# Optimization experiments

Measured on AMD Instinct MI355X. Metric: run time of the kernel, lower is better.

Reference implementation:

```python
import jax, jax.numpy as jnp
import numpy as np

# Model config (matches init_kwargs)
DIM = 2048
INTER = 1408          # moe_inter_dim
E = 16                # n_routed_experts
TOPK = 4              # n_activated_experts
G = 4                 # n_expert_groups
TOPK_G = 2            # n_limited_groups
N_SHARED = 2
SHARED_INTER = N_SHARED * INTER  # 2816
ROUTE_SCALE = 1.0


def setup_inputs() -> dict:
    key = jax.random.key(0)
    ks = jax.random.split(key, 8)
    s = 0.02
    x = jax.random.normal(ks[0], (1, 2048, DIM), dtype=jnp.float32)
    Wg = jax.random.normal(ks[1], (E, DIM), dtype=jnp.float32) * s      # gate weight
    W1 = jax.random.normal(ks[2], (E, INTER, DIM), dtype=jnp.float32) * s  # expert gate proj
    W3 = jax.random.normal(ks[3], (E, INTER, DIM), dtype=jnp.float32) * s  # expert up proj
    W2 = jax.random.normal(ks[4], (E, DIM, INTER), dtype=jnp.float32) * s  # expert down proj
    Ws1 = jax.random.normal(ks[5], (SHARED_INTER, DIM), dtype=jnp.float32) * s
    Ws3 = jax.random.normal(ks[6], (SHARED_INTER, DIM), dtype=jnp.float32) * s
    Ws2 = jax.random.normal(ks[7], (DIM, SHARED_INTER), dtype=jnp.float32) * s
    return {"x": x, "Wg": Wg, "W1": W1, "W3": W3, "W2": W2,
            "Ws1": Ws1, "Ws3": Ws3, "Ws2": Ws2}


def _moe_forward(x, Wg, W1, W3, W2, Ws1, Ws3, Ws2):
    B, S, D = x.shape
    xt = x.reshape(-1, D)              # [T, D]
    T = xt.shape[0]

    # ---- Gate: group-limited top-k routing (bias is None since dim != 7168) ----
    scores = jax.nn.softmax(xt @ Wg.T, axis=-1)          # [T, E]
    sg = scores.reshape(T, G, E // G)                    # [T, G, E/G]
    group_scores = sg.max(axis=-1)                       # amax per group
    gidx = jax.lax.top_k(group_scores, TOPK_G)[1]        # [T, TOPK_G]
    gmask = jax.nn.one_hot(gidx, G, dtype=jnp.float32).sum(axis=1) > 0  # [T, G] kept groups
    masked = jnp.where(gmask[:, :, None], sg, -jnp.inf).reshape(T, E)
    topi = jax.lax.top_k(masked, TOPK)[1]                # [T, TOPK] expert indices
    weights = jnp.take_along_axis(scores, topi, axis=1) * ROUTE_SCALE  # original_scores gather

    # ---- Routed experts: dense per-expert SwiGLU FFN, zero-weight combine ----
    # combine[t, e] = sum over k of weights[t, k] * (topi[t, k] == e)
    combine = jnp.zeros((T, E), xt.dtype).at[jnp.arange(T)[:, None], topi].add(weights)
    h = jax.nn.silu(jnp.einsum('td,eid->eti', xt, W1)) * jnp.einsum('td,eid->eti', xt, W3)
    expert_out = jnp.einsum('eti,edi->etd', h, W2)       # [E, T, D]
    y = jnp.einsum('etd,te->td', expert_out, combine)    # [T, D]

    # ---- Shared expert (applied to all tokens) ----
    z = (jax.nn.silu(xt @ Ws1.T) * (xt @ Ws3.T)) @ Ws2.T

    return (y + z).reshape(B, S, D)


def reference(x, Wg, W1, W3, W2, Ws1, Ws3, Ws2):
    return _moe_forward(x, Wg, W1, W3, W2, Ws1, Ws3, Ws2)
```

## Files before the change

kernel.cpp:

```cpp
#include <hip/hip_runtime.h>
#include <stdint.h>

#define D_MODEL  2048
#define N_INTER  1408
#define SH_INTER 2816
#define T_TOK    2048
#define NSLOT    (T_TOK * 4)
#define MIB(x)   ((size_t)(x) << 20)

typedef __attribute__((ext_vector_type(8))) short bf16x8;
typedef __attribute__((ext_vector_type(4))) float f32x4;

__device__ __forceinline__ unsigned short f2bf(float f){
  unsigned int b = __builtin_bit_cast(unsigned int, f);
  b = (b + 0x7FFFu + ((b >> 16) & 1u)) >> 16;
  return (unsigned short)b;
}
__device__ __forceinline__ float bf2f(unsigned short h){
  unsigned int b = ((unsigned int)h) << 16;
  return __builtin_bit_cast(float, b);
}

#define GLOAD16(gp, lp) __builtin_amdgcn_global_load_lds( \
    (const __attribute__((address_space(1))) unsigned int*)(gp), \
    (__attribute__((address_space(3))) unsigned int*)(lp), 16, 0, 0)

__global__ void cvt_bf16_kernel(const float* __restrict__ x,
                                unsigned short* __restrict__ o, int n4){
  const int stride = gridDim.x * blockDim.x;
  for (int i = blockIdx.x * blockDim.x + threadIdx.x; i < n4; i += stride){
    const float4 v = ((const float4*)x)[i];
    ushort4 u; u.x = f2bf(v.x); u.y = f2bf(v.y); u.z = f2bf(v.z); u.w = f2bf(v.w);
    ((ushort4*)o)[i] = u;
  }
}

__global__ void gate_kernel(const float* __restrict__ x, const float* __restrict__ Wg,
                            int* __restrict__ cnt, int* __restrict__ list,
                            float* __restrict__ wslot){
  const int t = blockIdx.x;
  const int l = threadIdx.x;
  const int e = l & 15, q = l >> 4;
  const float* xr = x + (size_t)t * D_MODEL + q * 512;
  const float* wr = Wg + (size_t)e * D_MODEL + q * 512;
  float p = 0.f;
  #pragma unroll 4
  for (int i = 0; i < 512; i += 4){
    float4 xv = *(const float4*)(xr + i);
    float4 wv = *(const float4*)(wr + i);
    p += xv.x*wv.x + xv.y*wv.y + xv.z*wv.z + xv.w*wv.w;
  }
  p += __shfl_xor(p, 16);
  p += __shfl_xor(p, 32);
  float mx = p;
  for (int d = 1; d < 16; d <<= 1) mx = fmaxf(mx, __shfl_xor(mx, d));
  float ex = __expf(p - mx);
  float sum = ex;
  for (int d = 1; d < 16; d <<= 1) sum += __shfl_xor(sum, d);
  const float sc = ex / sum;
  float gm = fmaxf(sc, __shfl_xor(sc, 1));
  gm = fmaxf(gm, __shfl_xor(gm, 2));
  const float g0 = __shfl(gm, 0), g1 = __shfl(gm, 4),
              g2 = __shfl(gm, 8), g3 = __shfl(gm, 12);
  const int grp = e >> 2;
  const float gs[4] = {g0, g1, g2, g3};
  int grank = 0;
  #pragma unroll
  for (int j = 0; j < 4; ++j)
    if (gs[j] > gm || (gs[j] == gm && j < grp)) grank++;
  const float msc = (grank < 2) ? sc : -INFINITY;
  int erank = 0;
  #pragma unroll
  for (int j = 0; j < 16; ++j){
    const float oj = __shfl(msc, j);
    if (oj > msc || (oj == msc && j < e)) erank++;
  }
  if (q == 0 && erank < 4 && msc > -INFINITY){
    const int pos = atomicAdd(&cnt[e], 1);
    const int slot = (t << 2) | erank;
    list[e * T_TOK + pos] = slot;
    wslot[slot] = sc;
  }
}

template<int MODE>
__global__ __launch_bounds__(256, 3)
void gemm6_kernel(const unsigned short* __restrict__ A,
                  const unsigned short* __restrict__ B,
                  void* __restrict__ OutP,
                  const int* __restrict__ list,
                  const int* __restrict__ cnt,
                  int N, int K, int Astride, int MT, int NT)
{
  constexpr bool GATHER = (MODE >= 2);
  __shared__ unsigned short As[3 * 128 * 32];
  __shared__ unsigned short Bs[3 * 128 * 32];

  const int per = gridDim.x >> 3;
  const int gsw = (blockIdx.x & 7) * per + (blockIdx.x >> 3);
  const int mt   = gsw % MT;
  const int rest = gsw / MT;
  const int nt = GATHER ? (rest % NT) : rest;
  const int e  = GATHER ? (rest / NT) : 0;

  const int cntE = GATHER ? cnt[e] : (MT * 128);
  if (mt * 128 >= cntE) return;

  const int tid = threadIdx.x, wid = tid >> 6, lane = tid & 63;

  const int rt0 = 32 * wid + (lane >> 2), rt1 = rt0 + 16;
  const int sxA = ((lane & 3) ^ ((lane >> 3) & 3)) << 3;

  int ar0, ar1;
  if constexpr (GATHER){
    const int lim = cntE - 1;
    int p0 = mt * 128 + rt0; p0 = p0 < lim ? p0 : lim;
    int p1 = mt * 128 + rt1; p1 = p1 < lim ? p1 : lim;
    const int e0 = list[e * T_TOK + p0], e1 = list[e * T_TOK + p1];
    ar0 = (MODE == 2) ? (e0 >> 2) : e0;
    ar1 = (MODE == 2) ? (e1 >> 2) : e1;
  } else { ar0 = mt * 128 + rt0; ar1 = mt * 128 + rt1; }

  const unsigned short* pa0 = A + (size_t)ar0 * Astride + sxA;
  const unsigned short* pa1 = A + (size_t)ar1 * Astride + sxA;
  const unsigned short* pb0 = B + (GATHER ? (size_t)e * N * K : 0)
                            + (size_t)(nt * 128 + rt0) * K + sxA;
  const unsigned short* pb1 = pb0 + (size_t)16 * K;

  const int aW0 = (32 * wid) * 32, aW1 = aW0 + 16 * 32;
  const int bufStride = 128 * 32;

  const int wr = wid >> 1, wc = wid & 1, lr = lane & 15, lq = lane >> 4;
  const int fx = ((lq ^ ((lr >> 1) & 3)) << 3);
  int aoff[4], boff[4];
  #pragma unroll
  for (int m = 0; m < 4; ++m) aoff[m] = (wr * 64 + m * 16 + lr) * 32 + fx;
  #pragma unroll
  for (int n = 0; n < 4; ++n) boff[n] = (wc * 64 + n * 16 + lr) * 32 + fx;

  f32x4 acc[4][4];
  const f32x4 zero = {0.f, 0.f, 0.f, 0.f};
  #pragma unroll
  for (int m = 0; m < 4; ++m)
    #pragma unroll
    for (int n = 0; n < 4; ++n) acc[m][n] = zero;

  const int KT = K >> 5;
  #pragma unroll
  for (int t = 0; t < 3; ++t){
    GLOAD16(pa0, As + t * bufStride + aW0);
    GLOAD16(pa1, As + t * bufStride + aW1);
    GLOAD16(pb0, Bs + t * bufStride + aW0);
    GLOAD16(pb1, Bs + t * bufStride + aW1);
    pa0 += 32; pa1 += 32; pb0 += 32; pb1 += 32;
  }
  int c = 0;

  for (int kt = 0; kt < KT; ++kt){
    if (kt < KT - 2)       asm volatile("s_waitcnt vmcnt(8)" ::: "memory");
    else if (kt == KT - 2) asm volatile("s_waitcnt vmcnt(4)" ::: "memory");
    else                   asm volatile("s_waitcnt vmcnt(0)" ::: "memory");
    __builtin_amdgcn_s_barrier();

    const unsigned short* aC = As + c * bufStride;
    const unsigned short* bC = Bs + c * bufStride;
    bf16x8 af[4], bf[4];
    #pragma unroll
    for (int m = 0; m < 4; ++m) af[m] = *(const bf16x8*)(aC + aoff[m]);
    #pragma unroll
    for (int n = 0; n < 4; ++n) bf[n] = *(const bf16x8*)(bC + boff[n]);

    asm volatile("s_waitcnt lgkmcnt(0)" ::: "memory");
    __builtin_amdgcn_sched_barrier(0);
    __builtin_amdgcn_s_barrier();

    if (kt + 3 < KT){
      GLOAD16(pa0, As + c * bufStride + aW0);
      GLOAD16(pa1, As + c * bufStride + aW1);
      GLOAD16(pb0, Bs + c * bufStride + aW0);
      GLOAD16(pb1, Bs + c * bufStride + aW1);
      pa0 += 32; pa1 += 32; pb0 += 32; pb1 += 32;
    }

    #pragma unroll
    for (int n = 0; n < 4; ++n)
      #pragma unroll
      for (int m = 0; m < 4; ++m)
        acc[m][n] = __builtin_amdgcn_mfma_f32_16x16x32_bf16(af[m], bf[n], acc[m][n], 0, 0, 0);

    c = (c == 2) ? 0 : c + 1;
  }

  const int colBase = nt * 128 + wc * 64;
  #pragma unroll
  for (int m = 0; m < 4; ++m){
    #pragma unroll
    for (int r = 0; r < 4; ++r){
      const int grow = mt * 128 + wr * 64 + m * 16 + lq * 4 + r;
      if constexpr (MODE == 1){
        float* op = (float*)OutP + (size_t)grow * N + colBase;
        #pragma unroll
        for (int n = 0; n < 4; ++n) op[n * 16 + lr] = acc[m][n][r];
      } else if constexpr (MODE == 0){
        unsigned short* op = (unsigned short*)OutP + (size_t)grow * N + colBase;
        #pragma unroll
        for (int n = 0; n < 4; ++n) op[n * 16 + lr] = f2bf(acc[m][n][r]);
      } else {
        if (grow >= cntE) continue;
        const int orow = list[e * T_TOK + grow];
        unsigned short* op = (unsigned short*)OutP + (size_t)orow * N + colBase;
        #pragma unroll
        for (int n = 0; n < 4; ++n) op[n * 16 + lr] = f2bf(acc[m][n][r]);
      }
    }
  }
}

__global__ void swiglu_ip_kernel(unsigned short* __restrict__ GU, int n8, int NI8){
  const int stride = gridDim.x * blockDim.x;
  bf16x8* p = (bf16x8*)GU;
  for (int i = blockIdx.x * blockDim.x + threadIdx.x; i < n8; i += stride){
    const int r = i / NI8, ccol = i - r * NI8;
    const size_t gi = (size_t)r * 2 * NI8 + ccol;
    const bf16x8 g = p[gi];
    const bf16x8 u = p[gi + NI8];
    bf16x8 h;
    #pragma unroll
    for (int j = 0; j < 8; ++j){
      const float gv = bf2f((unsigned short)g[j]);
      const float uv = bf2f((unsigned short)u[j]);
      h[j] = (short)f2bf(gv / (1.f + __expf(-gv)) * uv);
    }
    p[gi] = h;
  }
}

__global__ void swiglu2_kernel(unsigned short* __restrict__ G,
                               const unsigned short* __restrict__ U, int n8){
  const int stride = gridDim.x * blockDim.x;
  for (int i = blockIdx.x * blockDim.x + threadIdx.x; i < n8; i += stride){
    const bf16x8 g = ((const bf16x8*)G)[i];
    const bf16x8 u = ((const bf16x8*)U)[i];
    bf16x8 h;
    #pragma unroll
    for (int j = 0; j < 8; ++j){
      const float gv = bf2f((unsigned short)g[j]);
      const float uv = bf2f((unsigned short)u[j]);
      h[j] = (short)f2bf(gv / (1.f + __expf(-gv)) * uv);
    }
    ((bf16x8*)G)[i] = h;
  }
}

__global__ void combine_kernel(const unsigned short* __restrict__ H2,
                               const float* __restrict__ wslot,
                               float* __restrict__ out){
  const int t = blockIdx.x;
  const int ccol = threadIdx.x * 8;
  float w[4];
  #pragma unroll
  for (int k = 0; k < 4; ++k) w[k] = wslot[t * 4 + k];
  float* o = out + (size_t)t * D_MODEL + ccol;
  float a[8];
  #pragma unroll
  for (int j = 0; j < 8; ++j) a[j] = o[j];
  #pragma unroll
  for (int k = 0; k < 4; ++k){
    const bf16x8 hv = *(const bf16x8*)(H2 + (size_t)(t * 4 + k) * D_MODEL + ccol);
    #pragma unroll
    for (int j = 0; j < 8; ++j) a[j] += w[k] * bf2f((unsigned short)hv[j]);
  }
  #pragma unroll
  for (int j = 0; j < 8; ++j) o[j] = a[j];
}

extern "C" void kernel_launch(void* const* d_in, const int* in_sizes, int n_in,
                              void* d_out, int out_size, void* d_ws, size_t ws_size,
                              hipStream_t stream)
{
  const float* x   = (const float*)d_in[0];
  const float* Wg  = (const float*)d_in[1];
  const float* W1  = (const float*)d_in[2];
  const float* W3  = (const float*)d_in[3];
  const float* W2  = (const float*)d_in[4];
  const float* Ws1 = (const float*)d_in[5];
  const float* Ws3 = (const float*)d_in[6];
  const float* Ws2 = (const float*)d_in[7];
  float* out = (float*)d_out;

  char* ws = (char*)d_ws;
  int*   cnt   = (int*)(ws);
  int*   list  = (int*)(ws + 4096);
  float* wslot = (float*)(ws + 4096 + 131072);
  unsigned short* xbf  = (unsigned short*)(ws + MIB(1));
  unsigned short* H2   = (unsigned short*)(ws + MIB(1));
  unsigned short* GU_s = (unsigned short*)(ws + MIB(9));
  unsigned short* Ubuf = (unsigned short*)(ws + MIB(9));
  unsigned short* Wb   = (unsigned short*)(ws + MIB(33));
  unsigned short* Gbuf = (unsigned short*)(ws + MIB(121));
  unsigned short* Wb2  = Wb + (size_t)SH_INTER * D_MODEL;

  hipMemsetAsync(cnt, 0, 4096, stream);
  cvt_bf16_kernel<<<2048, 256, 0, stream>>>(x, xbf, T_TOK * D_MODEL / 4);
  gate_kernel<<<T_TOK, 64, 0, stream>>>(x, Wg, cnt, list, wslot);

  cvt_bf16_kernel<<<4096, 256, 0, stream>>>(Ws1, Wb,  SH_INTER * D_MODEL / 4);
  cvt_bf16_kernel<<<4096, 256, 0, stream>>>(Ws3, Wb2, SH_INTER * D_MODEL / 4);
  gemm6_kernel<0><<<16 * 44, 256, 0, stream>>>(xbf, Wb, GU_s, nullptr, nullptr,
                                               2 * SH_INTER, D_MODEL, D_MODEL, 16, 44);
  swiglu_ip_kernel<<<2048, 256, 0, stream>>>(GU_s, T_TOK * SH_INTER / 8, SH_INTER / 8);
  cvt_bf16_kernel<<<4096, 256, 0, stream>>>(Ws2, Wb, D_MODEL * SH_INTER / 4);
  gemm6_kernel<1><<<16 * 16, 256, 0, stream>>>(GU_s, Wb, out, nullptr, nullptr,
                                               D_MODEL, SH_INTER, 2 * SH_INTER, 16, 16);

  cvt_bf16_kernel<<<8192, 256, 0, stream>>>(W1, Wb, 16 * N_INTER * D_MODEL / 4);
  gemm6_kernel<2><<<16 * 11 * 16, 256, 0, stream>>>(xbf, Wb, Gbuf, list, cnt,
                                                    N_INTER, D_MODEL, D_MODEL, 16, 11);
  cvt_bf16_kernel<<<8192, 256, 0, stream>>>(W3, Wb, 16 * N_INTER * D_MODEL / 4);
  gemm6_kernel<2><<<16 * 11 * 16, 256, 0, stream>>>(xbf, Wb, Ubuf, list, cnt,
                                                    N_INTER, D_MODEL, D_MODEL, 16, 11);
  swiglu2_kernel<<<2048, 256, 0, stream>>>(Gbuf, Ubuf, NSLOT * N_INTER / 8);
  cvt_bf16_kernel<<<8192, 256, 0, stream>>>(W2, Wb, 16 * D_MODEL * N_INTER / 4);
  gemm6_kernel<3><<<16 * 16 * 16, 256, 0, stream>>>(Gbuf, Wb, H2, list, cnt,
                                                    D_MODEL, N_INTER, N_INTER, 16, 16);
  combine_kernel<<<T_TOK, 256, 0, stream>>>(H2, wslot, out);
}
```

Measured before the change: 604.5 us.

## Fuse gate/up GEMMs with SwiGLU epilogue and widen GEMM N-tiles to 256

Adds a gate/up GEMM kernel in which each block computes matching 128-column tiles of both the gate and up projections. The up tile is exchanged through shared memory and SiLU(g)*u is applied in the epilogue, so the separate SwiGLU kernels and the intermediate G/U buffer round trips go away. The down-projection GEMM now uses 128x256 tiles with 8 MFMA columns per wave. Routed expert weights are converted in two halves of 8 experts so W1 and W3 can sit in the workspace together. This raises register and LDS use per block (launch bounds drop to 2 blocks per CU) and halves the grid sizes, which may hurt occupancy and tail balance.

```diff
diff --git a/kernel.cpp b/kernel.cpp
--- a/kernel.cpp
+++ b/kernel.cpp
@@ -83,18 +83,169 @@
   }
 }
 
-template<int MODE>
-__global__ __launch_bounds__(256, 3)
-void gemm6_kernel(const unsigned short* __restrict__ A,
-                  const unsigned short* __restrict__ B,
-                  void* __restrict__ OutP,
-                  const int* __restrict__ list,
-                  const int* __restrict__ cnt,
-                  int N, int K, int Astride, int MT, int NT)
+template<int GATHER>
+__global__ __launch_bounds__(256, 2)
+void gemm_gu_kernel(const unsigned short* __restrict__ A,
+                    const unsigned short* __restrict__ BG,
+                    const unsigned short* __restrict__ BU,
+                    unsigned short* __restrict__ H,
+                    const int* __restrict__ list,
+                    const int* __restrict__ cnt,
+                    int ebase, int K, int NI, int MT, int NT)
 {
-  constexpr bool GATHER = (MODE >= 2);
-  __shared__ unsigned short As[3 * 128 * 32];
-  __shared__ unsigned short Bs[3 * 128 * 32];
+  __shared__ __align__(128) char smem[24576 + 49152];
+  unsigned short* As = (unsigned short*)smem;
+  unsigned short* Bs = (unsigned short*)(smem + 24576);
+  float* scr = (float*)smem;
+
+  const int per = gridDim.x >> 3;
+  const int gsw = (blockIdx.x & 7) * per + (blockIdx.x >> 3);
+  const int mt   = gsw % MT;
+  const int rest = gsw / MT;
+  const int nt = GATHER ? (rest % NT) : rest;
+  const int e  = GATHER ? (ebase + rest / NT) : 0;
+  const int cntE = GATHER ? cnt[e] : (MT * 128);
+  if (mt * 128 >= cntE) return;
+
+  const int tid = threadIdx.x, wid = tid >> 6, lane = tid & 63;
+  const int sx = ((lane & 3) ^ ((lane >> 3) & 3)) << 3;
+
+  const int rt0 = 32 * wid + (lane >> 2), rt1 = rt0 + 16;
+  int ar0, ar1;
+  if (GATHER){
+    const int lim = cntE - 1;
+    int p0 = mt * 128 + rt0; p0 = p0 < lim ? p0 : lim;
+    int p1 = mt * 128 + rt1; p1 = p1 < lim ? p1 : lim;
+    ar0 = list[e * T_TOK + p0] >> 2;
+    ar1 = list[e * T_TOK + p1] >> 2;
+  } else { ar0 = mt * 128 + rt0; ar1 = mt * 128 + rt1; }
+  const unsigned short* pa0 = A + (size_t)ar0 * K + sx;
+  const unsigned short* pa1 = A + (size_t)ar1 * K + sx;
+
+  const unsigned short* wsrc = (wid < 2) ? BG : BU;
+  if (GATHER) wsrc += (size_t)(e - ebase) * NI * K;
+  const int rb = (64 * wid + (lane >> 2)) & 127;
+  const unsigned short* pb0 = wsrc + (size_t)(nt * 128 + rb     ) * K + sx;
+  const unsigned short* pb1 = wsrc + (size_t)(nt * 128 + rb + 16) * K + sx;
+  const unsigned short* pb2 = wsrc + (size_t)(nt * 128 + rb + 32) * K + sx;
+  const unsigned short* pb3 = wsrc + (size_t)(nt * 128 + rb + 48) * K + sx;
+
+  const int aW0 = (32 * wid) * 32, aW1 = aW0 + 512;
+  const int bW  = (64 * wid) * 32;
+  const int aStr = 128 * 32, bStr = 256 * 32;
+
+  const int wr = wid >> 1, wc = wid & 1, lr = lane & 15, lq = lane >> 4;
+  const int fx = ((lq ^ ((lr >> 1) & 3)) << 3);
+  int aoff[4], boff[8];
+  #pragma unroll
+  for (int m = 0; m < 4; ++m) aoff[m] = (wr * 64 + m * 16 + lr) * 32 + fx;
+  #pragma unroll
+  for (int n = 0; n < 8; ++n) boff[n] = (wc * 128 + n * 16 + lr) * 32 + fx;
+
+  f32x4 acc[4][8];
+  const f32x4 zero = {0.f, 0.f, 0.f, 0.f};
+  #pragma unroll
+  for (int m = 0; m < 4; ++m)
+    #pragma unroll
+    for (int n = 0; n < 8; ++n) acc[m][n] = zero;
+
+  const int KT = K >> 5;
+  #pragma unroll
+  for (int t = 0; t < 3; ++t){
+    GLOAD16(pa0, As + t * aStr + aW0);
+    GLOAD16(pa1, As + t * aStr + aW1);
+    GLOAD16(pb0, Bs + t * bStr + bW);
+    GLOAD16(pb1, Bs + t * bStr + bW + 512);
+    GLOAD16(pb2, Bs + t * bStr + bW + 1024);
+    GLOAD16(pb3, Bs + t * bStr + bW + 1536);
+    pa0 += 32; pa1 += 32; pb0 += 32; pb1 += 32; pb2 += 32; pb3 += 32;
+  }
+  int c = 0;
+
+  for (int kt = 0; kt < KT; ++kt){
+    if (kt < KT - 2)       asm volatile("s_waitcnt vmcnt(12)" ::: "memory");
+    else if (kt == KT - 2) asm volatile("s_waitcnt vmcnt(6)"  ::: "memory");
+    else                   asm volatile("s_waitcnt vmcnt(0)"  ::: "memory");
+    __builtin_amdgcn_s_barrier();
+
+    const unsigned short* aC = As + c * aStr;
+    const unsigned short* bC = Bs + c * bStr;
+    bf16x8 af[4], bf[8];
+    #pragma unroll
+    for (int m = 0; m < 4; ++m) af[m] = *(const bf16x8*)(aC + aoff[m]);
+    #pragma unroll
+    for (int n = 0; n < 8; ++n) bf[n] = *(const bf16x8*)(bC + boff[n]);
+
+    asm volatile("s_waitcnt lgkmcnt(0)" ::: "memory");
+    __builtin_amdgcn_sched_barrier(0);
+    __builtin_amdgcn_s_barrier();
+
+    if (kt + 3 < KT){
+      GLOAD16(pa0, As + c * aStr + aW0);
+      GLOAD16(pa1, As + c * aStr + aW1);
+      GLOAD16(pb0, Bs + c * bStr + bW);
+      GLOAD16(pb1, Bs + c * bStr + bW + 512);
+      GLOAD16(pb2, Bs + c * bStr + bW + 1024);
+      GLOAD16(pb3, Bs + c * bStr + bW + 1536);
+      pa0 += 32; pa1 += 32; pb0 += 32; pb1 += 32; pb2 += 32; pb3 += 32;
+    }
+
+    #pragma unroll
+    for (int n = 0; n < 8; ++n)
+      #pragma unroll
+      for (int m = 0; m < 4; ++m)
+        acc[m][n] = __builtin_amdgcn_mfma_f32_16x16x32_bf16(af[m], bf[n], acc[m][n], 0, 0, 0);
+
+    c = (c == 2) ? 0 : c + 1;
+  }
+
+  if (wc == 1){
+    #pragma unroll
+    for (int m = 0; m < 4; ++m)
+      #pragma unroll
+      for (int r = 0; r < 4; ++r){
+        const int row = m * 16 + lq * 4 + r;
+        #pragma unroll
+        for (int n = 0; n < 8; ++n){
+          const int ucol = (n * 16 + lr) ^ ((lq & 1) << 4);
+          scr[wr * 8192 + row * 128 + ucol] = acc[m][n][r];
+        }
+      }
+  }
+  __syncthreads();
+  if (wc == 0){
+    #pragma unroll
+    for (int m = 0; m < 4; ++m)
+      #pragma unroll
+      for (int r = 0; r < 4; ++r){
+        const int row = m * 16 + lq * 4 + r;
+        const int grow = mt * 128 + wr * 64 + row;
+        if (GATHER && grow >= cntE) continue;
+        const int orow = GATHER ? list[e * T_TOK + grow] : grow;
+        unsigned short* op = H + (size_t)orow * NI + nt * 128;
+        #pragma unroll
+        for (int n = 0; n < 8; ++n){
+          const float g = acc[m][n][r];
+          const int ucol = (n * 16 + lr) ^ ((lq & 1) << 4);
+          const float u = scr[wr * 8192 + row * 128 + ucol];
+          op[n * 16 + lr] = f2bf(g / (1.f + __expf(-g)) * u);
+        }
+      }
+  }
+}
+
+template<int GATHER>
+__global__ __launch_bounds__(256, 2)
+void gemm_down_kernel(const unsigned short* __restrict__ A,
+                      const unsigned short* __restrict__ B,
+                      void* __restrict__ OutP,
+                      const int* __restrict__ list,
+                      const int* __restrict__ cnt,
+                      int K, int N, int MT, int NT)
+{
+  __shared__ __align__(128) char smem[24576 + 49152];
+  unsigned short* As = (unsigned short*)smem;
+  unsigned short* Bs = (unsigned short*)(smem + 24576);
 
   const int per = gridDim.x >> 3;
   const int gsw = (blockIdx.x & 7) * per + (blockIdx.x >> 3);
@@ -102,88 +253,93 @@
   const int rest = gsw / MT;
   const int nt = GATHER ? (rest % NT) : rest;
   const int e  = GATHER ? (rest / NT) : 0;
-
   const int cntE = GATHER ? cnt[e] : (MT * 128);
   if (mt * 128 >= cntE) return;
 
   const int tid = threadIdx.x, wid = tid >> 6, lane = tid & 63;
+  const int sx = ((lane & 3) ^ ((lane >> 3) & 3)) << 3;
 
   const int rt0 = 32 * wid + (lane >> 2), rt1 = rt0 + 16;
-  const int sxA = ((lane & 3) ^ ((lane >> 3) & 3)) << 3;
-
   int ar0, ar1;
-  if constexpr (GATHER){
+  if (GATHER){
     const int lim = cntE - 1;
     int p0 = mt * 128 + rt0; p0 = p0 < lim ? p0 : lim;
     int p1 = mt * 128 + rt1; p1 = p1 < lim ? p1 : lim;
-    const int e0 = list[e * T_TOK + p0], e1 = list[e * T_TOK + p1];
-    ar0 = (MODE == 2) ? (e0 >> 2) : e0;
-    ar1 = (MODE == 2) ? (e1 >> 2) : e1;
+    ar0 = list[e * T_TOK + p0];
+    ar1 = list[e * T_TOK + p1];
   } else { ar0 = mt * 128 + rt0; ar1 = mt * 128 + rt1; }
-
-  const unsigned short* pa0 = A + (size_t)ar0 * Astride + sxA;
-  const unsigned short* pa1 = A + (size_t)ar1 * Astride + sxA;
-  const unsigned short* pb0 = B + (GATHER ? (size_t)e * N * K : 0)
-                            + (size_t)(nt * 128 + rt0) * K + sxA;
-  const unsigned short* pb1 = pb0 + (size_t)16 * K;
-
-  const int aW0 = (32 * wid) * 32, aW1 = aW0 + 16 * 32;
-  const int bufStride = 128 * 32;
+  const unsigned short* pa0 = A + (size_t)ar0 * K + sx;
+  const unsigned short* pa1 = A + (size_t)ar1 * K + sx;
+
+  const unsigned short* wsrc = B + (GATHER ? (size_t)e * N * K : 0);
+  const int rb = 64 * wid + (lane >> 2);
+  const unsigned short* pb0 = wsrc + (size_t)(nt * 256 + rb     ) * K + sx;
+  const unsigned short* pb1 = wsrc + (size_t)(nt * 256 + rb + 16) * K + sx;
+  const unsigned short* pb2 = wsrc + (size_t)(nt * 256 + rb + 32) * K + sx;
+  const unsigned short* pb3 = wsrc + (size_t)(nt * 256 + rb + 48) * K + sx;
+
+  const int aW0 = (32 * wid) * 32, aW1 = aW0 + 512;
+  const int bW  = (64 * wid) * 32;
+  const int aStr = 128 * 32, bStr = 256 * 32;
 
   const int wr = wid >> 1, wc = wid & 1, lr = lane & 15, lq = lane >> 4;
   const int fx = ((lq ^ ((lr >> 1) & 3)) << 3);
-  int aoff[4], boff[4];
+  int aoff[4], boff[8];
   #pragma unroll
   for (int m = 0; m < 4; ++m) aoff[m] = (wr * 64 + m * 16 + lr) * 32 + fx;
   #pragma unroll
-  for (int n = 0; n < 4; ++n) boff[n] = (wc * 64 + n * 16 + lr) * 32 + fx;
-
-  f32x4 acc[4][4];
+  for (int n = 0; n < 8; ++n) boff[n] = (wc * 128 + n * 16 + lr) * 32 + fx;
+
+  f32x4 acc[4][8];
   const f32x4 zero = {0.f, 0.f, 0.f, 0.f};
   #pragma unroll
   for (int m = 0; m < 4; ++m)
     #pragma unroll
-    for (int n = 0; n < 4; ++n) acc[m][n] = zero;
+    for (int n = 0; n < 8; ++n) acc[m][n] = zero;
 
   const int KT = K >> 5;
   #pragma unroll
   for (int t = 0; t < 3; ++t){
-    GLOAD16(pa0, As + t * bufStride + aW0);
-    GLOAD16(pa1, As + t * bufStride + aW1);
-    GLOAD16(pb0, Bs + t * bufStride + aW0);
-    GLOAD16(pb1, Bs + t * bufStride + aW1);
-    pa0 += 32; pa1 += 32; pb0 += 32; pb1 += 32;
+    GLOAD16(pa0, As + t * aStr + aW0);
+    GLOAD16(pa1, As + t * aStr + aW1);
+    GLOAD16(pb0, Bs + t * bStr + bW);
+    GLOAD16(pb1, Bs + t * bStr + bW + 512);
+    GLOAD16(pb2, Bs + t * bStr + bW + 1024);
+    GLOAD16(pb3, Bs + t * bStr + bW + 1536);
+    pa0 += 32; pa1 += 32; pb0 += 32; pb1 += 32; pb2 += 32; pb3 += 32;
   }
   int c = 0;
 
   for (int kt = 0; kt < KT; ++kt){
-    if (kt < KT - 2)       asm volatile("s_waitcnt vmcnt(8)" ::: "memory");
-    else if (kt == KT - 2) asm volatile("s_waitcnt vmcnt(4)" ::: "memory");
-    else                   asm volatile("s_waitcnt vmcnt(0)" ::: "memory");
+    if (kt < KT - 2)       asm volatile("s_waitcnt vmcnt(12)" ::: "memory");
+    else if (kt == KT - 2) asm volatile("s_waitcnt vmcnt(6)"  ::: "memory");
+    else                   asm volatile("s_waitcnt vmcnt(0)"  ::: "memory");
     __builtin_amdgcn_s_barrier();
 
-    const unsigned short* aC = As + c * bufStride;
-    const unsigned short* bC = Bs + c * bufStride;
-    bf16x8 af[4], bf[4];
+    const unsigned short* aC = As + c * aStr;
+    const unsigned short* bC = Bs + c * bStr;
+    bf16x8 af[4], bf[8];
     #pragma unroll
     for (int m = 0; m < 4; ++m) af[m] = *(const bf16x8*)(aC + aoff[m]);
     #pragma unroll
-    for (int n = 0; n < 4; ++n) bf[n] = *(const bf16x8*)(bC + boff[n]);
+    for (int n = 0; n < 8; ++n) bf[n] = *(const bf16x8*)(bC + boff[n]);
 
     asm volatile("s_waitcnt lgkmcnt(0)" ::: "memory");
     __builtin_amdgcn_sched_barrier(0);
     __builtin_amdgcn_s_barrier();
 
     if (kt + 3 < KT){
-      GLOAD16(pa0, As + c * bufStride + aW0);
-      GLOAD16(pa1, As + c * bufStride + aW1);
-      GLOAD16(pb0, Bs + c * bufStride + aW0);
-      GLOAD16(pb1, Bs + c * bufStride + aW1);
-      pa0 += 32; pa1 += 32; pb0 += 32; pb1 += 32;
+      GLOAD16(pa0, As + c * aStr + aW0);
+      GLOAD16(pa1, As + c * aStr + aW1);
+      GLOAD16(pb0, Bs + c * bStr + bW);
+      GLOAD16(pb1, Bs + c * bStr + bW + 512);
+      GLOAD16(pb2, Bs + c * bStr + bW + 1024);
+      GLOAD16(pb3, Bs + c * bStr + bW + 1536);
+      pa0 += 32; pa1 += 32; pb0 += 32; pb1 += 32; pb2 += 32; pb3 += 32;
     }
 
     #pragma unroll
-    for (int n = 0; n < 4; ++n)
+    for (int n = 0; n < 8; ++n)
       #pragma unroll
       for (int m = 0; m < 4; ++m)
         acc[m][n] = __builtin_amdgcn_mfma_f32_16x16x32_bf16(af[m], bf[n], acc[m][n], 0, 0, 0);
@@ -191,64 +347,24 @@
     c = (c == 2) ? 0 : c + 1;
   }
 
-  const int colBase = nt * 128 + wc * 64;
+  const int colBase = nt * 256 + wc * 128;
   #pragma unroll
   for (int m = 0; m < 4; ++m){
     #pragma unroll
     for (int r = 0; r < 4; ++r){
       const int grow = mt * 128 + wr * 64 + m * 16 + lq * 4 + r;
-      if constexpr (MODE == 1){
+      if (GATHER == 0){
         float* op = (float*)OutP + (size_t)grow * N + colBase;
         #pragma unroll
-        for (int n = 0; n < 4; ++n) op[n * 16 + lr] = acc[m][n][r];
-      } else if constexpr (MODE == 0){
-        unsigned short* op = (unsigned short*)OutP + (size_t)grow * N + colBase;
-        #pragma unroll
-        for (int n = 0; n < 4; ++n) op[n * 16 + lr] = f2bf(acc[m][n][r]);
+        for (int n = 0; n < 8; ++n) op[n * 16 + lr] = acc[m][n][r];
       } else {
         if (grow >= cntE) continue;
         const int orow = list[e * T_TOK + grow];
         unsigned short* op = (unsigned short*)OutP + (size_t)orow * N + colBase;
         #pragma unroll
-        for (int n = 0; n < 4; ++n) op[n * 16 + lr] = f2bf(acc[m][n][r]);
+        for (int n = 0; n < 8; ++n) op[n * 16 + lr] = f2bf(acc[m][n][r]);
       }
     }
-  }
-}
-
-__global__ void swiglu_ip_kernel(unsigned short* __restrict__ GU, int n8, int NI8){
-  const int stride = gridDim.x * blockDim.x;
-  bf16x8* p = (bf16x8*)GU;
-  for (int i = blockIdx.x * blockDim.x + threadIdx.x; i < n8; i += stride){
-    const int r = i / NI8, ccol = i - r * NI8;
-    const size_t gi = (size_t)r * 2 * NI8 + ccol;
-    const bf16x8 g = p[gi];
-    const bf16x8 u = p[gi + NI8];
-    bf16x8 h;
-    #pragma unroll
-    for (int j = 0; j < 8; ++j){
-      const float gv = bf2f((unsigned short)g[j]);
-      const float uv = bf2f((unsigned short)u[j]);
-      h[j] = (short)f2bf(gv / (1.f + __expf(-gv)) * uv);
-    }
-    p[gi] = h;
-  }
-}
-
-__global__ void swiglu2_kernel(unsigned short* __restrict__ G,
-                               const unsigned short* __restrict__ U, int n8){
-  const int stride = gridDim.x * blockDim.x;
-  for (int i = blockIdx.x * blockDim.x + threadIdx.x; i < n8; i += stride){
-    const bf16x8 g = ((const bf16x8*)G)[i];
-    const bf16x8 u = ((const bf16x8*)U)[i];
-    bf16x8 h;
-    #pragma unroll
-    for (int j = 0; j < 8; ++j){
-      const float gv = bf2f((unsigned short)g[j]);
-      const float uv = bf2f((unsigned short)u[j]);
-      h[j] = (short)f2bf(gv / (1.f + __expf(-gv)) * uv);
-    }
-    ((bf16x8*)G)[i] = h;
   }
 }
 
@@ -292,36 +408,34 @@
   int*   cnt   = (int*)(ws);
   int*   list  = (int*)(ws + 4096);
   float* wslot = (float*)(ws + 4096 + 131072);
-  unsigned short* xbf  = (unsigned short*)(ws + MIB(1));
-  unsigned short* H2   = (unsigned short*)(ws + MIB(1));
-  unsigned short* GU_s = (unsigned short*)(ws + MIB(9));
-  unsigned short* Ubuf = (unsigned short*)(ws + MIB(9));
-  unsigned short* Wb   = (unsigned short*)(ws + MIB(33));
-  unsigned short* Gbuf = (unsigned short*)(ws + MIB(121));
-  unsigned short* Wb2  = Wb + (size_t)SH_INTER * D_MODEL;
+  unsigned short* xbf = (unsigned short*)(ws + MIB(1));
+  unsigned short* H2  = (unsigned short*)(ws + MIB(1));
+  unsigned short* Hs  = (unsigned short*)(ws + MIB(10));
+  unsigned short* Hr  = (unsigned short*)(ws + MIB(34));
+  unsigned short* WA  = (unsigned short*)(ws + MIB(57));
+  unsigned short* WB  = (unsigned short*)(ws + MIB(101));
 
   hipMemsetAsync(cnt, 0, 4096, stream);
   cvt_bf16_kernel<<<2048, 256, 0, stream>>>(x, xbf, T_TOK * D_MODEL / 4);
   gate_kernel<<<T_TOK, 64, 0, stream>>>(x, Wg, cnt, list, wslot);
 
-  cvt_bf16_kernel<<<4096, 256, 0, stream>>>(Ws1, Wb,  SH_INTER * D_MODEL / 4);
-  cvt_bf16_kernel<<<4096, 256, 0, stream>>>(Ws3, Wb2, SH_INTER * D_MODEL / 4);
-  gemm6_kernel<0><<<16 * 44, 256, 0, stream>>>(xbf, Wb, GU_s, nullptr, nullptr,
-                                               2 * SH_INTER, D_MODEL, D_MODEL, 16, 44);
-  swiglu_ip_kernel<<<2048, 256, 0, stream>>>(GU_s, T_TOK * SH_INTER / 8, SH_INTER / 8);
-  cvt_bf16_kernel<<<4096, 256, 0, stream>>>(Ws2, Wb, D_MODEL * SH_INTER / 4);
-  gemm6_kernel<1><<<16 * 16, 256, 0, stream>>>(GU_s, Wb, out, nullptr, nullptr,
-                                               D_MODEL, SH_INTER, 2 * SH_INTER, 16, 16);
-
-  cvt_bf16_kernel<<<8192, 256, 0, stream>>>(W1, Wb, 16 * N_INTER * D_MODEL / 4);
-  gemm6_kernel<2><<<16 * 11 * 16, 256, 0, stream>>>(xbf, Wb, Gbuf, list, cnt,
-                                                    N_INTER, D_MODEL, D_MODEL, 16, 11);
-  cvt_bf16_kernel<<<8192, 256, 0, stream>>>(W3, Wb, 16 * N_INTER * D_MODEL / 4);
-  gemm6_kernel<2><<<16 * 11 * 16, 256, 0, stream>>>(xbf, Wb, Ubuf, list, cnt,
-                                                    N_INTER, D_MODEL, D_MODEL, 16, 11);
-  swiglu2_kernel<<<2048, 256, 0, stream>>>(Gbuf, Ubuf, NSLOT * N_INTER / 8);
-  cvt_bf16_kernel<<<8192, 256, 0, stream>>>(W2, Wb, 16 * D_MODEL * N_INTER / 4);
-  gemm6_kernel<3><<<16 * 16 * 16, 256, 0, stream>>>(Gbuf, Wb, H2, list, cnt,
-                                                    D_MODEL, N_INTER, N_INTER, 16, 16);
+  cvt_bf16_kernel<<<2048, 256, 0, stream>>>(Ws1, WA, SH_INTER * D_MODEL / 4);
+  cvt_bf16_kernel<<<2048, 256, 0, stream>>>(Ws3, WB, SH_INTER * D_MODEL / 4);
+  gemm_gu_kernel<0><<<16 * 22, 256, 0, stream>>>(xbf, WA, WB, Hs, nullptr, nullptr,
+                                                 0, D_MODEL, SH_INTER, 16, 22);
+  cvt_bf16_kernel<<<2048, 256, 0, stream>>>(Ws2, WA, D_MODEL * SH_INTER / 4);
+  gemm_down_kernel<0><<<16 * 8, 256, 0, stream>>>(Hs, WA, out, nullptr, nullptr,
+                                                  SH_INTER, D_MODEL, 16, 8);
+
+  for (int h = 0; h < 2; ++h){
+    const size_t wOff = (size_t)(8 * h) * N_INTER * D_MODEL;
+    cvt_bf16_kernel<<<4096, 256, 0, stream>>>(W1 + wOff, WA, (int)(8u * N_INTER * D_MODEL / 4));
+    cvt_bf16_kernel<<<4096, 256, 0, stream>>>(W3 + wOff, WB, (int)(8u * N_INTER * D_MODEL / 4));
+    gemm_gu_kernel<1><<<16 * 11 * 8, 256, 0, stream>>>(xbf, WA, WB, Hr, list, cnt,
+                                                       8 * h, D_MODEL, N_INTER, 16, 11);
+  }
+  cvt_bf16_kernel<<<8192, 256, 0, stream>>>(W2, WA, 16 * D_MODEL * N_INTER / 4);
+  gemm_down_kernel<1><<<16 * 8 * 16, 256, 0, stream>>>(Hr, WA, H2, list, cnt,
+                                                       N_INTER, D_MODEL, 16, 8);
   combine_kernel<<<T_TOK, 256, 0, stream>>>(H2, wslot, out);
 }
```

Result: slower. 640.4 us (+5.9%).

## Overlap routed-expert weight conversion with GEMMs by appending convert blocks

Applied to the files above, without the earlier changes.

Merges the x and shared-expert weight fp32-to-bf16 conversions into one kernel. Each routed-expert weight conversion (W1, W3, W2) now runs as extra thread blocks appended to an earlier GEMM launch, so the memory-bound conversions run alongside compute-bound GEMM tiles instead of as separate serialized launches. The workspace layout gives each converted weight its own buffer, which uses much more scratch memory. The GEMM swizzle now uses the GEMM block count rather than the grid size, and conversion blocks may compete with GEMM tiles for CU slots.

```diff
diff --git a/kernel.cpp b/kernel.cpp
--- a/kernel.cpp
+++ b/kernel.cpp
@@ -25,13 +25,36 @@
     (const __attribute__((address_space(1))) unsigned int*)(gp), \
     (__attribute__((address_space(3))) unsigned int*)(lp), 16, 0, 0)
 
-__global__ void cvt_bf16_kernel(const float* __restrict__ x,
-                                unsigned short* __restrict__ o, int n4){
+__device__ __forceinline__ void cvt_tail(const float* __restrict__ src,
+                                         unsigned short* __restrict__ dst,
+                                         int n4, int cb, int nblk, int tid){
+  const float4* s = (const float4*)src;
+  ushort4* d = (ushort4*)dst;
+  const int stride = nblk * 256;
+  for (int i = cb * 256 + tid; i < n4; i += stride){
+    const float4 v = s[i];
+    ushort4 u; u.x = f2bf(v.x); u.y = f2bf(v.y); u.z = f2bf(v.z); u.w = f2bf(v.w);
+    d[i] = u;
+  }
+}
+
+__global__ void cvt4_kernel(const float* __restrict__ x,  const float* __restrict__ Ws1,
+                            const float* __restrict__ Ws3, const float* __restrict__ Ws2,
+                            unsigned short* __restrict__ xbf, unsigned short* __restrict__ S1,
+                            unsigned short* __restrict__ S3,  unsigned short* __restrict__ S2){
+  const int N0 = T_TOK * D_MODEL / 4;
+  const int NW = SH_INTER * D_MODEL / 4;
+  const int total = N0 + 3 * NW;
   const int stride = gridDim.x * blockDim.x;
-  for (int i = blockIdx.x * blockDim.x + threadIdx.x; i < n4; i += stride){
-    const float4 v = ((const float4*)x)[i];
+  for (int i = blockIdx.x * blockDim.x + threadIdx.x; i < total; i += stride){
+    const float4* s; ushort4* d; int j;
+    if (i < N0)            { s = (const float4*)x;   d = (ushort4*)xbf; j = i; }
+    else if (i < N0 + NW)  { s = (const float4*)Ws1; d = (ushort4*)S1;  j = i - N0; }
+    else if (i < N0 + 2*NW){ s = (const float4*)Ws3; d = (ushort4*)S3;  j = i - N0 - NW; }
+    else                   { s = (const float4*)Ws2; d = (ushort4*)S2;  j = i - N0 - 2*NW; }
+    const float4 v = s[j];
     ushort4 u; u.x = f2bf(v.x); u.y = f2bf(v.y); u.z = f2bf(v.z); u.w = f2bf(v.w);
-    ((ushort4*)o)[i] = u;
+    d[j] = u;
   }
 }
 
@@ -90,14 +113,24 @@
                   void* __restrict__ OutP,
                   const int* __restrict__ list,
                   const int* __restrict__ cnt,
-                  int N, int K, int Astride, int MT, int NT)
+                  int N, int K, int Astride, int MT, int NT,
+                  const float* __restrict__ cvtSrc,
+                  unsigned short* __restrict__ cvtDst,
+                  int cvtN4, int gemmN)
 {
   constexpr bool GATHER = (MODE >= 2);
   __shared__ unsigned short As[3 * 128 * 32];
   __shared__ unsigned short Bs[3 * 128 * 32];
 
-  const int per = gridDim.x >> 3;
-  const int gsw = (blockIdx.x & 7) * per + (blockIdx.x >> 3);
+  const int tid = threadIdx.x;
+  const int bid = blockIdx.x;
+  if (bid >= gemmN){
+    cvt_tail(cvtSrc, cvtDst, cvtN4, bid - gemmN, gridDim.x - gemmN, tid);
+    return;
+  }
+
+  const int per = gemmN >> 3;
+  const int gsw = (bid & 7) * per + (bid >> 3);
   const int mt   = gsw % MT;
   const int rest = gsw / MT;
   const int nt = GATHER ? (rest % NT) : rest;
@@ -106,7 +139,7 @@
   const int cntE = GATHER ? cnt[e] : (MT * 128);
   if (mt * 128 >= cntE) return;
 
-  const int tid = threadIdx.x, wid = tid >> 6, lane = tid & 63;
+  const int wid = tid >> 6, lane = tid & 63;
 
   const int rt0 = 32 * wid + (lane >> 2), rt1 = rt0 + 16;
   const int sxA = ((lane & 3) ^ ((lane >> 3) & 3)) << 3;
@@ -293,35 +326,45 @@
   int*   list  = (int*)(ws + 4096);
   float* wslot = (float*)(ws + 4096 + 131072);
   unsigned short* xbf  = (unsigned short*)(ws + MIB(1));
-  unsigned short* H2   = (unsigned short*)(ws + MIB(1));
-  unsigned short* GU_s = (unsigned short*)(ws + MIB(9));
-  unsigned short* Ubuf = (unsigned short*)(ws + MIB(9));
-  unsigned short* Wb   = (unsigned short*)(ws + MIB(33));
-  unsigned short* Gbuf = (unsigned short*)(ws + MIB(121));
-  unsigned short* Wb2  = Wb + (size_t)SH_INTER * D_MODEL;
+  unsigned short* S1   = (unsigned short*)(ws + MIB(10));
+  unsigned short* S3   = S1 + (size_t)SH_INTER * D_MODEL;
+  unsigned short* S2   = (unsigned short*)(ws + MIB(34));
+  unsigned short* GU_s = (unsigned short*)(ws + MIB(46));
+  unsigned short* Gbuf = (unsigned short*)(ws + MIB(70));
+  unsigned short* Ubuf = (unsigned short*)(ws + MIB(94));
+  unsigned short* H2   = (unsigned short*)(ws + MIB(118));
+  unsigned short* W1b  = (unsigned short*)(ws + MIB(152));
+  unsigned short* W3b  = (unsigned short*)(ws + MIB(245));
+  unsigned short* W2b  = (unsigned short*)(ws + MIB(338));
+
+  const int NW_R = 16 * N_INTER * D_MODEL / 4;
 
   hipMemsetAsync(cnt, 0, 4096, stream);
-  cvt_bf16_kernel<<<2048, 256, 0, stream>>>(x, xbf, T_TOK * D_MODEL / 4);
+  cvt4_kernel<<<2048, 256, 0, stream>>>(x, Ws1, Ws3, Ws2, xbf, S1, S3, S2);
   gate_kernel<<<T_TOK, 64, 0, stream>>>(x, Wg, cnt, list, wslot);
 
-  cvt_bf16_kernel<<<4096, 256, 0, stream>>>(Ws1, Wb,  SH_INTER * D_MODEL / 4);
-  cvt_bf16_kernel<<<4096, 256, 0, stream>>>(Ws3, Wb2, SH_INTER * D_MODEL / 4);
-  gemm6_kernel<0><<<16 * 44, 256, 0, stream>>>(xbf, Wb, GU_s, nullptr, nullptr,
-                                               2 * SH_INTER, D_MODEL, D_MODEL, 16, 44);
+  gemm6_kernel<0><<<704 + 1344, 256, 0, stream>>>(
+      xbf, S1, GU_s, nullptr, nullptr, 2 * SH_INTER, D_MODEL, D_MODEL, 16, 44,
+      W1, W1b, NW_R, 704);
   swiglu_ip_kernel<<<2048, 256, 0, stream>>>(GU_s, T_TOK * SH_INTER / 8, SH_INTER / 8);
-  cvt_bf16_kernel<<<4096, 256, 0, stream>>>(Ws2, Wb, D_MODEL * SH_INTER / 4);
-  gemm6_kernel<1><<<16 * 16, 256, 0, stream>>>(GU_s, Wb, out, nullptr, nullptr,
-                                               D_MODEL, SH_INTER, 2 * SH_INTER, 16, 16);
-
-  cvt_bf16_kernel<<<8192, 256, 0, stream>>>(W1, Wb, 16 * N_INTER * D_MODEL / 4);
-  gemm6_kernel<2><<<16 * 11 * 16, 256, 0, stream>>>(xbf, Wb, Gbuf, list, cnt,
-                                                    N_INTER, D_MODEL, D_MODEL, 16, 11);
-  cvt_bf16_kernel<<<8192, 256, 0, stream>>>(W3, Wb, 16 * N_INTER * D_MODEL / 4);
-  gemm6_kernel<2><<<16 * 11 * 16, 256, 0, stream>>>(xbf, Wb, Ubuf, list, cnt,
-                                                    N_INTER, D_MODEL, D_MODEL, 16, 11);
+
+  gemm6_kernel<1><<<256 + 1792, 256, 0, stream>>>(
+      GU_s, S2, out, nullptr, nullptr, D_MODEL, SH_INTER, 2 * SH_INTER, 16, 16,
+      W3, W3b, NW_R, 256);
+
+  gemm6_kernel<2><<<2816 + 1280, 256, 0, stream>>>(
+      xbf, W1b, Gbuf, list, cnt, N_INTER, D_MODEL, D_MODEL, 16, 11,
+      W2, W2b, NW_R, 2816);
+
+  gemm6_kernel<2><<<2816, 256, 0, stream>>>(
+      xbf, W3b, Ubuf, list, cnt, N_INTER, D_MODEL, D_MODEL, 16, 11,
+      nullptr, nullptr, 0, 2816);
+
   swiglu2_kernel<<<2048, 256, 0, stream>>>(Gbuf, Ubuf, NSLOT * N_INTER / 8);
-  cvt_bf16_kernel<<<8192, 256, 0, stream>>>(W2, Wb, 16 * D_MODEL * N_INTER / 4);
-  gemm6_kernel<3><<<16 * 16 * 16, 256, 0, stream>>>(Gbuf, Wb, H2, list, cnt,
-                                                    D_MODEL, N_INTER, N_INTER, 16, 16);
+
+  gemm6_kernel<3><<<4096, 256, 0, stream>>>(
+      Gbuf, W2b, H2, list, cnt, D_MODEL, N_INTER, N_INTER, 16, 16,
+      nullptr, nullptr, 0, 4096);
+
   combine_kernel<<<T_TOK, 256, 0, stream>>>(H2, wslot, out);
 }
```

After: 670.7 us. 1.11x slower.
